# Performance work log

Measured on AMD Instinct MI355X. Metric: run time of the kernel, lower is better.

The kernel has to match this reference:

```python
import jax, jax.numpy as jnp
import numpy as np

N_HEAD = 8


def setup_inputs() -> dict:
    key = jax.random.key(0)
    k1, k2, k3 = jax.random.split(key, 3)
    B, D, L = 4, 1024, 2048  # channels-first: (batch, feature, seq)
    q = jax.random.normal(k1, (B, D, L), dtype=jnp.float32)
    k = jax.random.normal(k2, (B, D, L), dtype=jnp.float32)
    v = jax.random.normal(k3, (B, D, L), dtype=jnp.float32)
    gamma = jnp.ones((), dtype=jnp.float32)  # nn.Parameter scalar, init 1.0
    return {"q": q, "k": k, "v": v, "gamma": gamma}


def reference(q, k, v, gamma):
    # q, k, v: (B, D, L) channels-first. Head split on feature dim (-2).
    B, Dq, Lq = q.shape
    Dv, Lk = v.shape[-2], v.shape[-1]
    h = N_HEAD
    dq = Dq // h  # per-head query/key dim
    dv = Dv // h  # per-head value dim
    qh = q.reshape(B, h, dq, Lq)
    kh = k.reshape(B, h, dq, Lk)
    vh = v.reshape(B, h, dv, Lk)
    # scale = sqrt(q.size(-2)) AFTER head split, i.e. sqrt(d_head)
    scale = 1.0 / jnp.sqrt(jnp.asarray(dq, dtype=q.dtype))
    # qk: (B, h, Lq, Lk)
    qk = jnp.einsum('bhdq,bhdl->bhql', qh, kh) * scale
    sm = jax.nn.softmax(qk, axis=-1)
    # torch: (sm.unsqueeze(-3) * v.unsqueeze(-2)).sum(-1) == contraction over Lk
    ret = jnp.einsum('bhql,bhdl->bhdq', sm, vh)  # (B, h, dv, Lq)
    ret = ret.reshape(B, Dv, Lq)  # torch: ret.view(-1, v_shape[-2], q_shape[-1])
    return gamma * ret
```

## Files before the change

kernel.cpp:

```cpp
#include <hip/hip_runtime.h>

#define SEQ 2048
#define DHEAD 128
#define BK 32
#define NBH 32

typedef __attribute__((ext_vector_type(8))) short bf16x8;
typedef __attribute__((ext_vector_type(4))) float f32x4;

__device__ __forceinline__ unsigned short f2bf(float f) {
    unsigned u = __builtin_bit_cast(unsigned, f);
    u += 0x7fffu + ((u >> 16) & 1u);
    return (unsigned short)(u >> 16);
}

__device__ __forceinline__ void gload16(const unsigned short* g, unsigned short* l) {
    __builtin_amdgcn_global_load_lds((const __attribute__((address_space(1))) void*)g,
                                     (__attribute__((address_space(3))) void*)l, 16, 0, 0);
}

__global__ __launch_bounds__(256)
void cvt_kernel(const float* __restrict__ kin, const float* __restrict__ vin,
                unsigned short* __restrict__ kout, unsigned short* __restrict__ vout) {
    const int tid = threadIdx.x;
    if (blockIdx.x < 1024) {
        __shared__ unsigned short tileT[DHEAD][66];
        const int bh = blockIdx.x & 31;
        const int l0 = (blockIdx.x >> 5) * 64;
        const float* ip = kin + (size_t)bh * DHEAD * SEQ;
        unsigned short* opx = kout + ((size_t)bh * SEQ + l0) * DHEAD;
        const int l4 = (tid & 15) * 4;
        const int dq = tid >> 4;
        for (int pass = 0; pass < 8; ++pass) {
            int d = pass * 16 + dq;
            float4 f = *(const float4*)&ip[(size_t)d * SEQ + l0 + l4];
            unsigned lo = (unsigned)f2bf(f.x) | ((unsigned)f2bf(f.y) << 16);
            unsigned hi = (unsigned)f2bf(f.z) | ((unsigned)f2bf(f.w) << 16);
            *(unsigned*)&tileT[d][l4]     = lo;
            *(unsigned*)&tileT[d][l4 + 2] = hi;
        }
        __syncthreads();
        const int lw = tid >> 2;
        const int cw = tid & 3;
        for (int j = 0; j < 4; ++j) {
            int pc = j * 4 + cw;
            int lc = pc ^ (lw & 7);
            unsigned short tmp[8];
            for (int k2 = 0; k2 < 8; ++k2) tmp[k2] = tileT[lc * 8 + k2][lw];
            *(bf16x8*)&opx[(size_t)lw * DHEAD + pc * 8] = *(bf16x8*)tmp;
        }
    } else {
        size_t f = ((size_t)(blockIdx.x - 1024) * 256 + tid) * 8;
        int bh  = (int)(f >> 18);
        int rem = (int)(f & 262143);
        int kt  = rem >> 12;
        int r2  = rem & 4095;
        int dv  = r2 >> 5;
        int e0  = r2 & 31;
        const float* src = vin + ((size_t)bh * DHEAD + dv) * SEQ + kt * BK + e0;
        float4 a = *(const float4*)src;
        float4 b = *(const float4*)(src + 4);
        unsigned short r[8] = {f2bf(a.x), f2bf(a.y), f2bf(a.z), f2bf(a.w),
                               f2bf(b.x), f2bf(b.y), f2bf(b.z), f2bf(b.w)};
        int pc = (e0 >> 3) ^ ((dv >> 1) & 3);
        size_t off = ((size_t)bh * (SEQ / BK) + kt) * (DHEAD * BK) + dv * BK + pc * 8;
        *(bf16x8*)&vout[off] = *(bf16x8*)r;
    }
}

__global__ __launch_bounds__(256, 2)
void attn_main(const float* __restrict__ q,
               const unsigned short* __restrict__ kTg,
               const unsigned short* __restrict__ vW,
               const float* __restrict__ gamma,
               float* __restrict__ out) {
    __shared__ unsigned short kS[2][BK * DHEAD];
    __shared__ unsigned short vS[2][DHEAD * BK];
    __shared__ unsigned short pS[4][16][40];

    const int tid  = threadIdx.x;
    const int wv   = tid >> 6;
    const int lane = tid & 63;
    const int c    = lane & 15;
    const int quad = lane >> 4;

    const int bh  = blockIdx.x & 31;
    const int qlb = blockIdx.x >> 5;
    const size_t base = (size_t)bh * SEQ * DHEAD;

    const float* qp = q + base;
    const unsigned short* kb = kTg + base;
    const unsigned short* vb = vW + base;
    float* op = out + base;

    const int ql0 = qlb * 128 + wv * 32;
    const float SCL = 0.08838834764831845f * 1.44269504088896340f;

    bf16x8 qf[2][4];
    for (int rs = 0; rs < 2; ++rs) {
        const int ql = ql0 + rs * 16 + c;
        for (int s = 0; s < 4; ++s) {
            bf16x8 fqs;
            for (int j = 0; j < 8; ++j)
                fqs[j] = (short)f2bf(qp[(size_t)(s * 32 + quad * 8 + j) * SEQ + ql] * SCL);
            qf[rs][s] = fqs;
        }
    }

    f32x4 accO[2][8];
    for (int rs = 0; rs < 2; ++rs)
        for (int t = 0; t < 8; ++t)
            accO[rs][t] = (f32x4){0.f, 0.f, 0.f, 0.f};
    float lp[2][4] = {{0.f,0.f,0.f,0.f},{0.f,0.f,0.f,0.f}};

    const int ksw = c & 7;
    const int vsw = (c >> 1) & 3;

    {
        gload16(kb + tid * 8,         &kS[0][tid * 8]);
        gload16(kb + (tid + 256) * 8, &kS[0][(tid + 256) * 8]);
        gload16(vb + tid * 8,         &vS[0][tid * 8]);
        gload16(vb + (tid + 256) * 8, &vS[0][(tid + 256) * 8]);
    }

    for (int kt = 0; kt < SEQ / BK; ++kt) {
        const int cur = kt & 1;
        __syncthreads();

        if (kt + 1 < SEQ / BK) {
            const unsigned short* kg = kb + (size_t)(kt + 1) * (BK * DHEAD);
            gload16(kg + tid * 8,         &kS[cur ^ 1][tid * 8]);
            gload16(kg + (tid + 256) * 8, &kS[cur ^ 1][(tid + 256) * 8]);
            const unsigned short* vg = vb + (size_t)(kt + 1) * (DHEAD * BK);
            gload16(vg + tid * 8,         &vS[cur ^ 1][tid * 8]);
            gload16(vg + (tid + 256) * 8, &vS[cur ^ 1][(tid + 256) * 8]);
        }

        bf16x8 kf0[4], kf1[4];
        for (int s = 0; s < 4; ++s) {
            int pc = (4 * s + quad) ^ ksw;
            kf0[s] = *(const bf16x8*)&kS[cur][c * DHEAD + pc * 8];
            kf1[s] = *(const bf16x8*)&kS[cur][(16 + c) * DHEAD + pc * 8];
        }
        bf16x8 vf[8];
        for (int t = 0; t < 8; ++t)
            vf[t] = *(const bf16x8*)&vS[cur][(t * 16 + c) * BK + ((quad ^ vsw) * 8)];

        for (int rs = 0; rs < 2; ++rs) {
            f32x4 s0 = (f32x4){0.f, 0.f, 0.f, 0.f};
            f32x4 s1 = (f32x4){0.f, 0.f, 0.f, 0.f};
            for (int s = 0; s < 4; ++s) {
                s0 = __builtin_amdgcn_mfma_f32_16x16x32_bf16(qf[rs][s], kf0[s], s0, 0, 0, 0);
                s1 = __builtin_amdgcn_mfma_f32_16x16x32_bf16(qf[rs][s], kf1[s], s1, 0, 0, 0);
            }

            for (int r = 0; r < 4; ++r) {
                float p0 = exp2f(s0[r]);
                float p1 = exp2f(s1[r]);
                lp[rs][r] += p0 + p1;
                pS[wv][4 * quad + r][c]      = f2bf(p0);
                pS[wv][4 * quad + r][16 + c] = f2bf(p1);
            }
            asm volatile("s_waitcnt lgkmcnt(0)" ::: "memory");

            bf16x8 bp = *(const bf16x8*)&pS[wv][c][quad * 8];
            for (int t = 0; t < 8; ++t)
                accO[rs][t] = __builtin_amdgcn_mfma_f32_16x16x32_bf16(vf[t], bp, accO[rs][t], 0, 0, 0);
        }
    }

    const float gm = gamma[0];
    for (int rs = 0; rs < 2; ++rs) {
        float L[4];
        for (int r = 0; r < 4; ++r) {
            float s = lp[rs][r];
            s += __shfl_xor(s, 1, 16);
            s += __shfl_xor(s, 2, 16);
            s += __shfl_xor(s, 4, 16);
            s += __shfl_xor(s, 8, 16);
            L[r] = s;
        }
        int srcl = (c >> 2) << 4;
        float L0 = __shfl(L[0], srcl);
        float L1 = __shfl(L[1], srcl);
        float L2 = __shfl(L[2], srcl);
        float L3 = __shfl(L[3], srcl);
        int rsel = c & 3;
        float lsel = rsel == 0 ? L0 : rsel == 1 ? L1 : rsel == 2 ? L2 : L3;
        float sc = gm / lsel;
        int ql = ql0 + rs * 16 + c;
        for (int t = 0; t < 8; ++t)
            for (int r = 0; r < 4; ++r)
                op[(size_t)(t * 16 + quad * 4 + r) * SEQ + ql] = accO[rs][t][r] * sc;
    }
}

extern "C" void kernel_launch(void* const* d_in, const int* in_sizes, int n_in,
                              void* d_out, int out_size, void* d_ws, size_t ws_size,
                              hipStream_t stream) {
    (void)in_sizes; (void)n_in; (void)out_size; (void)ws_size;
    const float* q = (const float*)d_in[0];
    const float* k = (const float*)d_in[1];
    const float* v = (const float*)d_in[2];
    const float* g = (const float*)d_in[3];
    float* out = (float*)d_out;

    const size_t PER_T = (size_t)NBH * SEQ * DHEAD;
    unsigned short* kws = (unsigned short*)d_ws;
    unsigned short* vws = kws + PER_T;

    cvt_kernel<<<dim3(1024 + 4096), dim3(256), 0, stream>>>(k, v, kws, vws);
    attn_main<<<dim3(512), dim3(256), 0, stream>>>(q, kws, vws, g, out);
}
```

Measured before the change: 228.9 us.

## Switch attention to 32x32x16 MFMA with transposed scores kept in registers

```diff
diff --git a/kernel.cpp b/kernel.cpp
--- a/kernel.cpp
+++ b/kernel.cpp
@@ -6,7 +6,9 @@
 #define NBH 32
 
 typedef __attribute__((ext_vector_type(8))) short bf16x8;
-typedef __attribute__((ext_vector_type(4))) float f32x4;
+typedef __attribute__((ext_vector_type(4))) short bf16x4;
+typedef __attribute__((ext_vector_type(16))) float f32x16;
+typedef __attribute__((ext_vector_type(4))) unsigned int u32x4;
 
 __device__ __forceinline__ unsigned short f2bf(float f) {
     unsigned u = __builtin_bit_cast(unsigned, f);
@@ -60,11 +62,14 @@
         const float* src = vin + ((size_t)bh * DHEAD + dv) * SEQ + kt * BK + e0;
         float4 a = *(const float4*)src;
         float4 b = *(const float4*)(src + 4);
-        unsigned short r[8] = {f2bf(a.x), f2bf(a.y), f2bf(a.z), f2bf(a.w),
-                               f2bf(b.x), f2bf(b.y), f2bf(b.z), f2bf(b.w)};
-        int pc = (e0 >> 3) ^ ((dv >> 1) & 3);
-        size_t off = ((size_t)bh * (SEQ / BK) + kt) * (DHEAD * BK) + dv * BK + pc * 8;
-        *(bf16x8*)&vout[off] = *(bf16x8*)r;
+        unsigned short p0[4] = {f2bf(a.x), f2bf(a.y), f2bf(a.z), f2bf(a.w)};
+        unsigned short p1[4] = {f2bf(b.x), f2bf(b.y), f2bf(b.z), f2bf(b.w)};
+        const int aa = e0 >> 4;
+        const int bb = (e0 >> 3) & 1;
+        const int w  = (dv >> 1) & 3;
+        size_t rowb = ((size_t)bh * (SEQ / BK) + kt) * (DHEAD * BK) + (size_t)dv * BK;
+        *(bf16x4*)&vout[rowb + (size_t)(((2 * aa) ^ w) * 8 + 4 * bb)]     = *(bf16x4*)p0;
+        *(bf16x4*)&vout[rowb + (size_t)(((2 * aa + 1) ^ w) * 8 + 4 * bb)] = *(bf16x4*)p1;
     }
 }
 
@@ -74,15 +79,14 @@
                const unsigned short* __restrict__ vW,
                const float* __restrict__ gamma,
                float* __restrict__ out) {
-    __shared__ unsigned short kS[2][BK * DHEAD];
-    __shared__ unsigned short vS[2][DHEAD * BK];
-    __shared__ unsigned short pS[4][16][40];
+    __shared__ __attribute__((aligned(16))) unsigned short kS[2][BK * DHEAD];
+    __shared__ __attribute__((aligned(16))) unsigned short vS[2][DHEAD * BK];
 
     const int tid  = threadIdx.x;
     const int wv   = tid >> 6;
     const int lane = tid & 63;
-    const int c    = lane & 15;
-    const int quad = lane >> 4;
+    const int c5   = lane & 31;
+    const int hi   = lane >> 5;
 
     const int bh  = blockIdx.x & 31;
     const int qlb = blockIdx.x >> 5;
@@ -93,35 +97,33 @@
     const unsigned short* vb = vW + base;
     float* op = out + base;
 
-    const int ql0 = qlb * 128 + wv * 32;
+    const int ql = qlb * 128 + wv * 32 + c5;
     const float SCL = 0.08838834764831845f * 1.44269504088896340f;
 
-    bf16x8 qf[2][4];
-    for (int rs = 0; rs < 2; ++rs) {
-        const int ql = ql0 + rs * 16 + c;
-        for (int s = 0; s < 4; ++s) {
-            bf16x8 fqs;
-            for (int j = 0; j < 8; ++j)
-                fqs[j] = (short)f2bf(qp[(size_t)(s * 32 + quad * 8 + j) * SEQ + ql] * SCL);
-            qf[rs][s] = fqs;
-        }
+    gload16(kb + tid * 8,         &kS[0][tid * 8]);
+    gload16(kb + (tid + 256) * 8, &kS[0][(tid + 256) * 8]);
+    gload16(vb + tid * 8,         &vS[0][tid * 8]);
+    gload16(vb + (tid + 256) * 8, &vS[0][(tid + 256) * 8]);
+
+    bf16x8 qf[8];
+#pragma unroll
+    for (int s = 0; s < 8; ++s) {
+        bf16x8 t;
+#pragma unroll
+        for (int j = 0; j < 8; ++j)
+            t[j] = (short)f2bf(qp[(size_t)(s * 16 + hi * 8 + j) * SEQ + ql] * SCL);
+        qf[s] = t;
     }
 
-    f32x4 accO[2][8];
-    for (int rs = 0; rs < 2; ++rs)
-        for (int t = 0; t < 8; ++t)
-            accO[rs][t] = (f32x4){0.f, 0.f, 0.f, 0.f};
-    float lp[2][4] = {{0.f,0.f,0.f,0.f},{0.f,0.f,0.f,0.f}};
-
-    const int ksw = c & 7;
-    const int vsw = (c >> 1) & 3;
-
-    {
-        gload16(kb + tid * 8,         &kS[0][tid * 8]);
-        gload16(kb + (tid + 256) * 8, &kS[0][(tid + 256) * 8]);
-        gload16(vb + tid * 8,         &vS[0][tid * 8]);
-        gload16(vb + (tid + 256) * 8, &vS[0][(tid + 256) * 8]);
-    }
+    f32x16 accO[4];
+#pragma unroll
+    for (int t = 0; t < 4; ++t)
+#pragma unroll
+        for (int i = 0; i < 16; ++i) accO[t][i] = 0.f;
+    float lp = 0.f;
+
+    const int ksw = c5 & 7;
+    const int vsw = (c5 >> 1) & 3;
 
     for (int kt = 0; kt < SEQ / BK; ++kt) {
         const int cur = kt & 1;
@@ -136,63 +138,52 @@
             gload16(vg + (tid + 256) * 8, &vS[cur ^ 1][(tid + 256) * 8]);
         }
 
-        bf16x8 kf0[4], kf1[4];
-        for (int s = 0; s < 4; ++s) {
-            int pc = (4 * s + quad) ^ ksw;
-            kf0[s] = *(const bf16x8*)&kS[cur][c * DHEAD + pc * 8];
-            kf1[s] = *(const bf16x8*)&kS[cur][(16 + c) * DHEAD + pc * 8];
-        }
-        bf16x8 vf[8];
-        for (int t = 0; t < 8; ++t)
-            vf[t] = *(const bf16x8*)&vS[cur][(t * 16 + c) * BK + ((quad ^ vsw) * 8)];
-
-        for (int rs = 0; rs < 2; ++rs) {
-            f32x4 s0 = (f32x4){0.f, 0.f, 0.f, 0.f};
-            f32x4 s1 = (f32x4){0.f, 0.f, 0.f, 0.f};
-            for (int s = 0; s < 4; ++s) {
-                s0 = __builtin_amdgcn_mfma_f32_16x16x32_bf16(qf[rs][s], kf0[s], s0, 0, 0, 0);
-                s1 = __builtin_amdgcn_mfma_f32_16x16x32_bf16(qf[rs][s], kf1[s], s1, 0, 0, 0);
-            }
-
-            for (int r = 0; r < 4; ++r) {
-                float p0 = exp2f(s0[r]);
-                float p1 = exp2f(s1[r]);
-                lp[rs][r] += p0 + p1;
-                pS[wv][4 * quad + r][c]      = f2bf(p0);
-                pS[wv][4 * quad + r][16 + c] = f2bf(p1);
-            }
-            asm volatile("s_waitcnt lgkmcnt(0)" ::: "memory");
-
-            bf16x8 bp = *(const bf16x8*)&pS[wv][c][quad * 8];
-            for (int t = 0; t < 8; ++t)
-                accO[rs][t] = __builtin_amdgcn_mfma_f32_16x16x32_bf16(vf[t], bp, accO[rs][t], 0, 0, 0);
+        bf16x8 kf[8], vf[8];
+#pragma unroll
+        for (int s = 0; s < 8; ++s)
+            kf[s] = *(const bf16x8*)&kS[cur][c5 * DHEAD + (((2 * s + hi) ^ ksw) * 8)];
+#pragma unroll
+        for (int t = 0; t < 4; ++t)
+#pragma unroll
+            for (int s2 = 0; s2 < 2; ++s2)
+                vf[t * 2 + s2] = *(const bf16x8*)&vS[cur][(32 * t + c5) * BK + (((2 * s2 + hi) ^ vsw) * 8)];
+
+        f32x16 sT;
+#pragma unroll
+        for (int i = 0; i < 16; ++i) sT[i] = 0.f;
+#pragma unroll
+        for (int s = 0; s < 8; ++s)
+            sT = __builtin_amdgcn_mfma_f32_32x32x16_bf16(kf[s], qf[s], sT, 0, 0, 0);
+
+        unsigned pw[8];
+#pragma unroll
+        for (int i = 0; i < 8; ++i) {
+            float pa = exp2f(sT[2 * i]);
+            float pb = exp2f(sT[2 * i + 1]);
+            lp += pa + pb;
+            unsigned r;
+            asm("v_cvt_pk_bf16_f32 %0, %1, %2" : "=v"(r) : "v"(pa), "v"(pb));
+            pw[i] = r;
+        }
+        bf16x8 pf0 = __builtin_bit_cast(bf16x8, (u32x4){pw[0], pw[1], pw[2], pw[3]});
+        bf16x8 pf1 = __builtin_bit_cast(bf16x8, (u32x4){pw[4], pw[5], pw[6], pw[7]});
+
+#pragma unroll
+        for (int t = 0; t < 4; ++t) {
+            accO[t] = __builtin_amdgcn_mfma_f32_32x32x16_bf16(vf[t * 2],     pf0, accO[t], 0, 0, 0);
+            accO[t] = __builtin_amdgcn_mfma_f32_32x32x16_bf16(vf[t * 2 + 1], pf1, accO[t], 0, 0, 0);
         }
     }
 
-    const float gm = gamma[0];
-    for (int rs = 0; rs < 2; ++rs) {
-        float L[4];
-        for (int r = 0; r < 4; ++r) {
-            float s = lp[rs][r];
-            s += __shfl_xor(s, 1, 16);
-            s += __shfl_xor(s, 2, 16);
-            s += __shfl_xor(s, 4, 16);
-            s += __shfl_xor(s, 8, 16);
-            L[r] = s;
-        }
-        int srcl = (c >> 2) << 4;
-        float L0 = __shfl(L[0], srcl);
-        float L1 = __shfl(L[1], srcl);
-        float L2 = __shfl(L[2], srcl);
-        float L3 = __shfl(L[3], srcl);
-        int rsel = c & 3;
-        float lsel = rsel == 0 ? L0 : rsel == 1 ? L1 : rsel == 2 ? L2 : L3;
-        float sc = gm / lsel;
-        int ql = ql0 + rs * 16 + c;
-        for (int t = 0; t < 8; ++t)
-            for (int r = 0; r < 4; ++r)
-                op[(size_t)(t * 16 + quad * 4 + r) * SEQ + ql] = accO[rs][t][r] * sc;
-    }
+    const float L = lp + __shfl_xor(lp, 32);
+    const float sc = gamma[0] / L;
+#pragma unroll
+    for (int t = 0; t < 4; ++t)
+#pragma unroll
+        for (int r = 0; r < 16; ++r) {
+            int dvr = 32 * t + (r & 3) + 8 * (r >> 2) + 4 * hi;
+            op[(size_t)dvr * SEQ + ql] = accO[t][r] * sc;
+        }
 }
 
 extern "C" void kernel_launch(void* const* d_in, const int* in_sizes, int n_in,
```

After: 211.5 us. 7.6% less time.
